# Performance work log

Measured on AMD Instinct MI355X. Metric: run time of the kernel, lower is better.

## Reference

```python
import jax, jax.numpy as jnp
import numpy as np

B, T, C, H = 2, 2048, 1024, 16
HD = C // H  # head dim = 64


def setup_inputs() -> dict:
    key = jax.random.key(0)
    ks = jax.random.split(key, 5)
    scale = 0.02
    return {
        "x": jax.random.normal(ks[0], (B, T, C), dtype=jnp.float32),
        "W_attn": jax.random.normal(ks[1], (C, 3 * C), dtype=jnp.float32) * scale,
        "b_attn": jax.random.normal(ks[2], (3 * C,), dtype=jnp.float32) * scale,
        "W_proj": jax.random.normal(ks[3], (C, C), dtype=jnp.float32) * scale,
        "b_proj": jax.random.normal(ks[4], (C,), dtype=jnp.float32) * scale,
    }


def reference(x, W_attn, b_attn, W_proj, b_proj):
    Bd, Td, Cd = x.shape
    qkv = x @ W_attn + b_attn                      # [B,T,3C]
    q, k, v = jnp.split(qkv, 3, axis=-1)           # each [B,T,C]
    # [B,T,C] -> [B,H,T,HD]
    def heads(t):
        return t.reshape(Bd, Td, H, HD).transpose(0, 2, 1, 3)
    q, k, v = heads(q), heads(k), heads(v)
    att = jnp.einsum('bhqd,bhkd->bhqk', q, k) * (1.0 / np.sqrt(HD))
    causal = jnp.tril(jnp.ones((Td, Td), dtype=bool))
    att = jnp.where(causal[None, None, :, :], att, -jnp.inf)
    att = jax.nn.softmax(att, axis=-1)
    y = jnp.einsum('bhqk,bhkd->bhqd', att, v)      # [B,H,T,HD]
    y = y.transpose(0, 2, 1, 3).reshape(Bd, Td, Cd)
    return y @ W_proj + b_proj
```

## Files before the change

### kernel.cpp

```cpp
#include <hip/hip_runtime.h>
#include <hip/hip_bf16.h>


typedef __attribute__((ext_vector_type(8))) __bf16 bf16x8;
typedef __attribute__((ext_vector_type(8))) short short8;
typedef __attribute__((ext_vector_type(4))) short short4v;
typedef __attribute__((ext_vector_type(4))) float floatx4;

__device__ __forceinline__ unsigned short f2b(float f) {
    unsigned int x = __float_as_uint(f);
    x += 0x7fffu + ((x >> 16) & 1u);
    return (unsigned short)(x >> 16);
}
__device__ __forceinline__ unsigned short f2b_trunc(float f) {
    return (unsigned short)(__float_as_uint(f) >> 16);
}
__device__ __forceinline__ void gld16(const void* g, void* l) {
    __builtin_amdgcn_global_load_lds((const __attribute__((address_space(1))) void*)g,
                                     (__attribute__((address_space(3))) void*)l, 16, 0, 0);
}

__global__ __launch_bounds__(256) void prep_k(
    const float* __restrict__ x,  unsigned short* __restrict__ xb,
    const float* __restrict__ Wa, unsigned short* __restrict__ WTa,
    const float* __restrict__ Wp, unsigned short* __restrict__ WTp)
{
    __shared__ unsigned short tl[64][72];
    const int id = blockIdx.x, t = threadIdx.x;

    if (id < 2048) {
        int i = (id * 256 + t) << 3;
        const float4 a = *(const float4*)(x + i);
        const float4 b = *(const float4*)(x + i + 4);
        short8 v;
        v[0] = (short)f2b(a.x); v[1] = (short)f2b(a.y);
        v[2] = (short)f2b(a.z); v[3] = (short)f2b(a.w);
        v[4] = (short)f2b(b.x); v[5] = (short)f2b(b.y);
        v[6] = (short)f2b(b.z); v[7] = (short)f2b(b.w);
        *(short8*)(xb + i) = v;
        return;
    }

    const float* in;
    unsigned short* out;
    int R, Cc, bx, by;
    if (id < 2816) {
        in = Wa; out = WTa; R = 1024; Cc = 3072;
        bx = (id - 2048) % 48; by = (id - 2048) / 48;
    } else {
        in = Wp; out = WTp; R = 1024; Cc = 1024;
        bx = (id - 2816) % 16; by = (id - 2816) / 16;
    }
    const int r0 = by * 64, c0 = bx * 64;
#pragma unroll
    for (int it = 0; it < 2; ++it) {
        int idx = it * 256 + t, r = idx >> 3, c8 = (idx & 7) << 3;
        const float* p = in + (size_t)(r0 + r) * Cc + c0 + c8;
        const float4 a = *(const float4*)p;
        const float4 b = *(const float4*)(p + 4);
        tl[r][c8 + 0] = f2b(a.x); tl[r][c8 + 1] = f2b(a.y);
        tl[r][c8 + 2] = f2b(a.z); tl[r][c8 + 3] = f2b(a.w);
        tl[r][c8 + 4] = f2b(b.x); tl[r][c8 + 5] = f2b(b.y);
        tl[r][c8 + 6] = f2b(b.z); tl[r][c8 + 7] = f2b(b.w);
    }
    __syncthreads();
#pragma unroll
    for (int it = 0; it < 2; ++it) {
        int idx = it * 256 + t, rr = idx >> 3, c8 = (idx & 7) << 3;
        short8 v;
#pragma unroll
        for (int i = 0; i < 8; ++i) v[i] = (short)tl[c8 + i][rr];
        *(short8*)(out + (size_t)(c0 + rr) * R + r0 + c8) = v;
    }
}

__global__ __launch_bounds__(256) void gemm_qkv(
    const unsigned short* __restrict__ A,
    const unsigned short* __restrict__ BT,
    const float* __restrict__ bias,
    unsigned short* __restrict__ outqk,
    unsigned short* __restrict__ outvt)
{
    __shared__ __align__(16) unsigned short SM[2][2][128][32];
    unsigned short* Esc = &SM[0][0][0][0];

    const int t = threadIdx.x;
    const int w = t >> 6, lane = t & 63, l15 = lane & 15, quad = lane >> 4;
    const int wr = w >> 1, wc = w & 1;
    const int m0 = blockIdx.y * 128, n0 = blockIdx.x * 128;
    const int K = 1024;

    float bia[4];
#pragma unroll
    for (int j = 0; j < 4; ++j) bia[j] = bias[n0 + wc * 64 + j * 16 + l15];

    floatx4 acc[4][4];
#pragma unroll
    for (int i = 0; i < 4; ++i)
#pragma unroll
        for (int j = 0; j < 4; ++j) acc[i][j] = (floatx4)0.f;

    const int row_s = t >> 2, kg_s = (t & 3) << 3;
    const unsigned short* gA = A  + (size_t)(m0 + row_s) * K + kg_s;
    const unsigned short* gB = BT + (size_t)(n0 + row_s) * K + kg_s;
    const int ldst = (w * 64) * 8;

#pragma unroll
    for (int c = 0; c < 2; ++c) {
        gld16(gA + (size_t)c * 64 * K, &SM[0][0][0][0] + c * 2048 + ldst);
        gld16(gB + (size_t)c * 64 * K, &SM[0][1][0][0] + c * 2048 + ldst);
    }

    for (int it = 0; it < 32; ++it) {
        __syncthreads();
        const int cur = it & 1;
        if (it < 31) {
            const int k0 = (it + 1) * 32;
#pragma unroll
            for (int c = 0; c < 2; ++c) {
                gld16(gA + (size_t)c * 64 * K + k0, &SM[cur ^ 1][0][0][0] + c * 2048 + ldst);
                gld16(gB + (size_t)c * 64 * K + k0, &SM[cur ^ 1][1][0][0] + c * 2048 + ldst);
            }
        }
        bf16x8 af[4], bfr[4];
#pragma unroll
        for (int i = 0; i < 4; ++i) af[i] = *(const bf16x8*)&SM[cur][0][wr * 64 + i * 16 + l15][quad * 8];
#pragma unroll
        for (int j = 0; j < 4; ++j) bfr[j] = *(const bf16x8*)&SM[cur][1][wc * 64 + j * 16 + l15][quad * 8];
#pragma unroll
        for (int i = 0; i < 4; ++i)
#pragma unroll
            for (int j = 0; j < 4; ++j)
                acc[i][j] = __builtin_amdgcn_mfma_f32_16x16x32_bf16(af[i], bfr[j], acc[i][j], 0, 0, 0);
    }

    const int bb = m0 >> 11, tbase = m0 & 2047;
    if (n0 < 2048) {
        for (int cf = 0; cf < 2; ++cf) {
            const int fb = n0 + cf * 64;
            const int which = fb >> 10, h = (fb & 1023) >> 6;
            const float scl = (which == 0) ? 0.18033688011112042f : 1.0f;
            __syncthreads();
            if (wc == cf) {
#pragma unroll
                for (int i = 0; i < 4; ++i)
#pragma unroll
                    for (int j = 0; j < 4; ++j)
#pragma unroll
                        for (int r = 0; r < 4; ++r)
                            Esc[(wr * 64 + i * 16 + quad * 4 + r) * 72 + j * 16 + l15] =
                                f2b((acc[i][j][r] + bia[j]) * scl);
            }
            __syncthreads();
            const int row = t >> 1, co = (t & 1) << 5;
            const unsigned short* src = Esc + row * 72 + co;
            unsigned short* dst = outqk + (size_t)which * 4194304
                + (((size_t)(bb * 16 + h) * 2048 + tbase + row) * 64 + co);
#pragma unroll
            for (int u = 0; u < 4; ++u)
                *(short8*)(dst + u * 8) = *(const short8*)(src + u * 8);
        }
    } else {
        const int hb = (n0 & 1023) >> 6;
        for (int hf = 0; hf < 2; ++hf) {
            __syncthreads();
            if (wr == hf) {
#pragma unroll
                for (int i = 0; i < 4; ++i)
#pragma unroll
                    for (int j = 0; j < 4; ++j) {
                        short4v pk;
#pragma unroll
                        for (int r = 0; r < 4; ++r) pk[r] = (short)f2b(acc[i][j][r] + bia[j]);
                        *(short4v*)&Esc[(wc * 64 + j * 16 + l15) * 72 + i * 16 + quad * 4] = pk;
                    }
            }
            __syncthreads();
            const int dl = t >> 1, co = (t & 1) << 5;
            const int h = hb + (dl >> 6), d = dl & 63;
            const unsigned short* src = Esc + dl * 72 + co;
            unsigned short* dst = outvt
                + (((size_t)(bb * 16 + h) * 64 + d) * 2048 + tbase + hf * 64 + co);
#pragma unroll
            for (int u = 0; u < 4; ++u)
                *(short8*)(dst + u * 8) = *(const short8*)(src + u * 8);
        }
    }
}

__global__ __launch_bounds__(256) void gemm_proj(
    const unsigned short* __restrict__ A,
    const unsigned short* __restrict__ BT,
    const float* __restrict__ bias,
    float* __restrict__ outf)
{
    __shared__ __align__(16) unsigned short SM[2][2][128][32];
    float* Ef = (float*)&SM[0][0][0][0];

    const int t = threadIdx.x;
    const int w = t >> 6, lane = t & 63, l15 = lane & 15, quad = lane >> 4;
    const int wr = w >> 1, wc = w & 1;
    const int m0 = blockIdx.y * 128, n0 = blockIdx.x * 128;
    const int K = 1024, N = 1024;

    float bia[4];
#pragma unroll
    for (int j = 0; j < 4; ++j) bia[j] = bias[n0 + wc * 64 + j * 16 + l15];

    floatx4 acc[4][4];
#pragma unroll
    for (int i = 0; i < 4; ++i)
#pragma unroll
        for (int j = 0; j < 4; ++j) acc[i][j] = (floatx4)0.f;

    const int row_s = t >> 2, kg_s = (t & 3) << 3;
    const unsigned short* gA = A  + (size_t)(m0 + row_s) * K + kg_s;
    const unsigned short* gB = BT + (size_t)(n0 + row_s) * K + kg_s;
    const int ldst = (w * 64) * 8;

#pragma unroll
    for (int c = 0; c < 2; ++c) {
        gld16(gA + (size_t)c * 64 * K, &SM[0][0][0][0] + c * 2048 + ldst);
        gld16(gB + (size_t)c * 64 * K, &SM[0][1][0][0] + c * 2048 + ldst);
    }

    for (int it = 0; it < 32; ++it) {
        __syncthreads();
        const int cur = it & 1;
        if (it < 31) {
            const int k0 = (it + 1) * 32;
#pragma unroll
            for (int c = 0; c < 2; ++c) {
                gld16(gA + (size_t)c * 64 * K + k0, &SM[cur ^ 1][0][0][0] + c * 2048 + ldst);
                gld16(gB + (size_t)c * 64 * K + k0, &SM[cur ^ 1][1][0][0] + c * 2048 + ldst);
            }
        }
        bf16x8 af[4], bfr[4];
#pragma unroll
        for (int i = 0; i < 4; ++i) af[i] = *(const bf16x8*)&SM[cur][0][wr * 64 + i * 16 + l15][quad * 8];
#pragma unroll
        for (int j = 0; j < 4; ++j) bfr[j] = *(const bf16x8*)&SM[cur][1][wc * 64 + j * 16 + l15][quad * 8];
#pragma unroll
        for (int i = 0; i < 4; ++i)
#pragma unroll
            for (int j = 0; j < 4; ++j)
                acc[i][j] = __builtin_amdgcn_mfma_f32_16x16x32_bf16(af[i], bfr[j], acc[i][j], 0, 0, 0);
    }

    for (int qf = 0; qf < 4; ++qf) {
        __syncthreads();
        if (wr == (qf >> 1)) {
            const int ib = (qf & 1) * 2;
#pragma unroll
            for (int ii = 0; ii < 2; ++ii)
#pragma unroll
                for (int j = 0; j < 4; ++j)
#pragma unroll
                    for (int r = 0; r < 4; ++r)
                        Ef[(ii * 16 + quad * 4 + r) * 132 + wc * 64 + j * 16 + l15] =
                            acc[ib + ii][j][r] + bia[j];
        }
        __syncthreads();
        const int row = t >> 3, co = (t & 7) << 4;
        const float* src = Ef + row * 132 + co;
        float* dst = outf + (size_t)(m0 + qf * 32 + row) * N + n0 + co;
#pragma unroll
        for (int u = 0; u < 4; ++u)
            *(float4*)(dst + u * 4) = *(const float4*)(src + u * 4);
    }
}

__global__ __launch_bounds__(256) void attn_k(
    const unsigned short* __restrict__ qg,
    const unsigned short* __restrict__ kg,
    const unsigned short* __restrict__ vt,
    unsigned short* __restrict__ y)
{
    __shared__ unsigned short Kb[2][64][64];
    __shared__ unsigned short Vb[2][64][64];
    __shared__ unsigned short Pld[4][16][72];

    const int t = threadIdx.x, w = t >> 6, lane = t & 63;
    const int l15 = lane & 15, quad = lane >> 4;
    const int id = blockIdx.x;
    const int bh = (id & 7) * 4 + ((id >> 3) & 3);
    const int p = id >> 5;
    const int b = bh >> 4, h = bh & 15;

    bf16x8 ones;
#pragma unroll
    for (int i = 0; i < 8; ++i) ones[i] = (__bf16)1.0f;

    const int r_s = t >> 3;
    const int g_s = t & 7;

#pragma unroll 1
    for (int hv = 0; hv < 2; ++hv) {
        const int qt = hv ? (31 - p) : p;
        const int qbase = qt * 64;

        bf16x8 qa[2];
        {
            const unsigned short* qrow = qg + ((size_t)bh * 2048 + qbase + w * 16 + l15) * 64;
            qa[0] = *(const bf16x8*)(qrow + quad * 8);
            qa[1] = *(const bf16x8*)(qrow + 32 + quad * 8);
        }

        floatx4 O[4];
#pragma unroll
        for (int j = 0; j < 4; ++j) O[j] = (floatx4)0.f;
        floatx4 lacc = (floatx4)0.f;

        __syncthreads();
        {
#pragma unroll
            for (int c = 0; c < 2; ++c) {
                int r = c * 32 + r_s;
                int cg = (g_s ^ (r & 7)) << 3;
                gld16(kg + ((size_t)bh * 2048 + r) * 64 + cg,
                      &Kb[0][0][0] + (size_t)(c * 256 + w * 64) * 8);
                gld16(vt + ((size_t)bh * 64 + r) * 2048 + cg,
                      &Vb[0][0][0] + (size_t)(c * 256 + w * 64) * 8);
            }
        }

#pragma unroll 1
        for (int kt = 0; kt <= qt; ++kt) {
            __syncthreads();
            const int cur = kt & 1;
            if (kt < qt) {
                const int kbase = (kt + 1) * 64, nxt = cur ^ 1;
#pragma unroll
                for (int c = 0; c < 2; ++c) {
                    int r = c * 32 + r_s;
                    int cg = (g_s ^ (r & 7)) << 3;
                    gld16(kg + ((size_t)bh * 2048 + kbase + r) * 64 + cg,
                          &Kb[nxt][0][0] + (size_t)(c * 256 + w * 64) * 8);
                    gld16(vt + ((size_t)bh * 64 + r) * 2048 + kbase + cg,
                          &Vb[nxt][0][0] + (size_t)(c * 256 + w * 64) * 8);
                }
            }

            floatx4 sv[4];
#pragma unroll
            for (int jn = 0; jn < 4; ++jn) sv[jn] = (floatx4)0.f;
#pragma unroll
            for (int kk = 0; kk < 2; ++kk) {
#pragma unroll
                for (int jn = 0; jn < 4; ++jn) {
                    bf16x8 bfr = *(const bf16x8*)&Kb[cur][jn * 16 + l15][((kk * 4 + quad) ^ (l15 & 7)) << 3];
                    sv[jn] = __builtin_amdgcn_mfma_f32_16x16x32_bf16(qa[kk], bfr, sv[jn], 0, 0, 0);
                }
            }

            if (kt == qt) {
#pragma unroll
                for (int jn = 0; jn < 4; ++jn) {
                    int key = jn * 16 + l15;
#pragma unroll
                    for (int r = 0; r < 4; ++r) {
                        int qr = w * 16 + quad * 4 + r;
                        sv[jn][r] = exp2f((key > qr) ? -1e30f : sv[jn][r]);
                    }
                }
            } else {
#pragma unroll
                for (int jn = 0; jn < 4; ++jn)
#pragma unroll
                    for (int r = 0; r < 4; ++r) sv[jn][r] = exp2f(sv[jn][r]);
            }

#pragma unroll
            for (int jn = 0; jn < 4; ++jn)
#pragma unroll
                for (int r = 0; r < 4; ++r)
                    Pld[w][quad * 4 + r][jn * 16 + l15] = f2b_trunc(sv[jn][r]);
            __builtin_amdgcn_wave_barrier();
            __builtin_amdgcn_s_waitcnt(0xc07f);
            __builtin_amdgcn_wave_barrier();

#pragma unroll
            for (int kk = 0; kk < 2; ++kk) {
                bf16x8 pa = *(const bf16x8*)&Pld[w][l15][kk * 32 + quad * 8];
                lacc = __builtin_amdgcn_mfma_f32_16x16x32_bf16(pa, ones, lacc, 0, 0, 0);
#pragma unroll
                for (int jd = 0; jd < 4; ++jd) {
                    bf16x8 vb = *(const bf16x8*)&Vb[cur][jd * 16 + l15][((kk * 4 + quad) ^ (l15 & 7)) << 3];
                    O[jd] = __builtin_amdgcn_mfma_f32_16x16x32_bf16(pa, vb, O[jd], 0, 0, 0);
                }
            }
        }

#pragma unroll
        for (int r = 0; r < 4; ++r) {
            float inv = 1.f / lacc[r];
            int tt = qbase + w * 16 + quad * 4 + r;
#pragma unroll
            for (int jd = 0; jd < 4; ++jd) {
                int c = h * 64 + jd * 16 + l15;
                y[((size_t)b * 2048 + tt) * 1024 + c] = f2b(O[jd][r] * inv);
            }
        }
    }
}

extern "C" void kernel_launch(void* const* d_in, const int* in_sizes, int n_in,
                              void* d_out, int out_size, void* d_ws, size_t ws_size,
                              hipStream_t stream) {
    const float* x      = (const float*)d_in[0];
    const float* W_attn = (const float*)d_in[1];
    const float* b_attn = (const float*)d_in[2];
    const float* W_proj = (const float*)d_in[3];
    const float* b_proj = (const float*)d_in[4];
    float* out = (float*)d_out;

    char* ws = (char*)d_ws;
    unsigned short* qk  = (unsigned short*)(ws);
    unsigned short* vtb = (unsigned short*)(ws + 16777216);
    unsigned short* y   = (unsigned short*)(ws + 25165824);
    unsigned short* xb  = (unsigned short*)(ws + 33554432);
    unsigned short* WTa = (unsigned short*)(ws + 41943040);
    unsigned short* WTp = (unsigned short*)(ws + 48234496);

    prep_k<<<3072, 256, 0, stream>>>(x, xb, W_attn, WTa, W_proj, WTp);
    gemm_qkv<<<dim3(24, 32), 256, 0, stream>>>(xb, WTa, b_attn, qk, vtb);
    attn_k<<<512, 256, 0, stream>>>(qk, qk + 4194304, vtb, y);
    gemm_proj<<<dim3(8, 32), 256, 0, stream>>>(y, WTp, b_proj, out);
}
```

Before: 201.1 us.

## Transpose attention scores into registers and run PV in fp16 MFMA

The attention kernel now computes the transposed score tile K·Q^T, so the exponentiated probabilities already sit in the register layout the PV MFMA needs. This removes the per-wave LDS staging buffer and its wait. P and V switch to fp16 with the 16x16x16 f16 MFMA, and the QKV kernel now writes V as fp16 using round-toward-zero pack conversion. Each block now covers 128 contiguous query rows instead of a pair of mirrored 64-row tiles, with the largest-work blocks launched first. The trade-offs are smaller-K MFMAs, a different precision profile for P·V, and possible load imbalance across blocks.

```diff
diff --git a/kernel.cpp b/kernel.cpp
--- a/kernel.cpp
+++ b/kernel.cpp
@@ -6,14 +6,19 @@
 typedef __attribute__((ext_vector_type(8))) short short8;
 typedef __attribute__((ext_vector_type(4))) short short4v;
 typedef __attribute__((ext_vector_type(4))) float floatx4;
+typedef __attribute__((ext_vector_type(2))) __fp16 fp16x2;
+typedef __attribute__((ext_vector_type(4))) _Float16 half4v;
 
 __device__ __forceinline__ unsigned short f2b(float f) {
     unsigned int x = __float_as_uint(f);
     x += 0x7fffu + ((x >> 16) & 1u);
     return (unsigned short)(x >> 16);
 }
-__device__ __forceinline__ unsigned short f2b_trunc(float f) {
-    return (unsigned short)(__float_as_uint(f) >> 16);
+__device__ __forceinline__ half4v pack4h(float a, float b, float c, float d) {
+    union { fp16x2 c2[2]; half4v h4; } u;
+    u.c2[0] = __builtin_amdgcn_cvt_pkrtz(a, b);
+    u.c2[1] = __builtin_amdgcn_cvt_pkrtz(c, d);
+    return u.h4;
 }
 __device__ __forceinline__ void gld16(const void* g, void* l) {
     __builtin_amdgcn_global_load_lds((const __attribute__((address_space(1))) void*)g,
@@ -169,10 +174,9 @@
                 for (int i = 0; i < 4; ++i)
 #pragma unroll
                     for (int j = 0; j < 4; ++j) {
-                        short4v pk;
-#pragma unroll
-                        for (int r = 0; r < 4; ++r) pk[r] = (short)f2b(acc[i][j][r] + bia[j]);
-                        *(short4v*)&Esc[(wc * 64 + j * 16 + l15) * 72 + i * 16 + quad * 4] = pk;
+                        half4v hp = pack4h(acc[i][j][0] + bia[j], acc[i][j][1] + bia[j],
+                                           acc[i][j][2] + bia[j], acc[i][j][3] + bia[j]);
+                        *(half4v*)&Esc[(wc * 64 + j * 16 + l15) * 72 + i * 16 + quad * 4] = hp;
                     }
             }
             __syncthreads();
@@ -278,128 +282,113 @@
 {
     __shared__ unsigned short Kb[2][64][64];
     __shared__ unsigned short Vb[2][64][64];
-    __shared__ unsigned short Pld[4][16][72];
 
     const int t = threadIdx.x, w = t >> 6, lane = t & 63;
     const int l15 = lane & 15, quad = lane >> 4;
     const int id = blockIdx.x;
-    const int bh = (id & 7) * 4 + ((id >> 3) & 3);
-    const int p = id >> 5;
+    const int s = id >> 3;
+    const int bh = (id & 7) * 4 + (s & 3);
+    const int p = 15 - (s >> 2);
     const int b = bh >> 4, h = bh & 15;
-
-    bf16x8 ones;
-#pragma unroll
-    for (int i = 0; i < 8; ++i) ones[i] = (__bf16)1.0f;
-
-    const int r_s = t >> 3;
-    const int g_s = t & 7;
+    const int q0 = p * 128 + w * 32;
+    const int ktend = 2 * p + 2;
+
+    const half4v onesh = {(_Float16)1.f, (_Float16)1.f, (_Float16)1.f, (_Float16)1.f};
+
+    bf16x8 Qf[2][2];
+#pragma unroll
+    for (int qb = 0; qb < 2; ++qb) {
+        const unsigned short* qrow = qg + ((size_t)bh * 2048 + q0 + qb * 16 + l15) * 64 + quad * 8;
+        Qf[qb][0] = *(const bf16x8*)(qrow);
+        Qf[qb][1] = *(const bf16x8*)(qrow + 32);
+    }
+
+    floatx4 OT[2][4];
+#pragma unroll
+    for (int qb = 0; qb < 2; ++qb)
+#pragma unroll
+        for (int jd = 0; jd < 4; ++jd) OT[qb][jd] = (floatx4)0.f;
+    floatx4 lacc[2];
+    lacc[0] = (floatx4)0.f; lacc[1] = (floatx4)0.f;
+
+    const int r_s = t >> 3, g_s = t & 7;
+
+#pragma unroll
+    for (int c = 0; c < 2; ++c) {
+        int r = c * 32 + r_s;
+        int cg = (g_s ^ (r & 7)) << 3;
+        gld16(kg + ((size_t)bh * 2048 + r) * 64 + cg, &Kb[0][0][0] + (size_t)(c * 256 + w * 64) * 8);
+        gld16(vt + ((size_t)bh * 64 + r) * 2048 + cg, &Vb[0][0][0] + (size_t)(c * 256 + w * 64) * 8);
+    }
 
 #pragma unroll 1
-    for (int hv = 0; hv < 2; ++hv) {
-        const int qt = hv ? (31 - p) : p;
-        const int qbase = qt * 64;
-
-        bf16x8 qa[2];
-        {
-            const unsigned short* qrow = qg + ((size_t)bh * 2048 + qbase + w * 16 + l15) * 64;
-            qa[0] = *(const bf16x8*)(qrow + quad * 8);
-            qa[1] = *(const bf16x8*)(qrow + 32 + quad * 8);
-        }
-
-        floatx4 O[4];
-#pragma unroll
-        for (int j = 0; j < 4; ++j) O[j] = (floatx4)0.f;
-        floatx4 lacc = (floatx4)0.f;
-
+    for (int kt = 0; kt < ktend; ++kt) {
         __syncthreads();
-        {
+        const int cur = kt & 1;
+        if (kt + 1 < ktend) {
+            const int kbase = (kt + 1) * 64, nxt = cur ^ 1;
 #pragma unroll
             for (int c = 0; c < 2; ++c) {
                 int r = c * 32 + r_s;
                 int cg = (g_s ^ (r & 7)) << 3;
-                gld16(kg + ((size_t)bh * 2048 + r) * 64 + cg,
-                      &Kb[0][0][0] + (size_t)(c * 256 + w * 64) * 8);
-                gld16(vt + ((size_t)bh * 64 + r) * 2048 + cg,
-                      &Vb[0][0][0] + (size_t)(c * 256 + w * 64) * 8);
-            }
-        }
-
-#pragma unroll 1
-        for (int kt = 0; kt <= qt; ++kt) {
-            __syncthreads();
-            const int cur = kt & 1;
-            if (kt < qt) {
-                const int kbase = (kt + 1) * 64, nxt = cur ^ 1;
-#pragma unroll
-                for (int c = 0; c < 2; ++c) {
-                    int r = c * 32 + r_s;
-                    int cg = (g_s ^ (r & 7)) << 3;
-                    gld16(kg + ((size_t)bh * 2048 + kbase + r) * 64 + cg,
-                          &Kb[nxt][0][0] + (size_t)(c * 256 + w * 64) * 8);
-                    gld16(vt + ((size_t)bh * 64 + r) * 2048 + kbase + cg,
-                          &Vb[nxt][0][0] + (size_t)(c * 256 + w * 64) * 8);
+                gld16(kg + ((size_t)bh * 2048 + kbase + r) * 64 + cg,
+                      &Kb[nxt][0][0] + (size_t)(c * 256 + w * 64) * 8);
+                gld16(vt + ((size_t)bh * 64 + r) * 2048 + kbase + cg,
+                      &Vb[nxt][0][0] + (size_t)(c * 256 + w * 64) * 8);
+            }
+        }
+
+#pragma unroll
+        for (int jk = 0; jk < 4; ++jk) {
+            bf16x8 Kf0 = *(const bf16x8*)&Kb[cur][jk * 16 + l15][((0 * 4 + quad) ^ (l15 & 7)) << 3];
+            bf16x8 Kf1 = *(const bf16x8*)&Kb[cur][jk * 16 + l15][((1 * 4 + quad) ^ (l15 & 7)) << 3];
+            half4v Vf[4];
+#pragma unroll
+            for (int jd = 0; jd < 4; ++jd) {
+                const int pc = ((((2 * jk) + (quad >> 1)) ^ (l15 & 7)) << 3) + (quad & 1) * 4;
+                Vf[jd] = *(const half4v*)&Vb[cur][jd * 16 + l15][pc];
+            }
+
+#pragma unroll
+            for (int qb = 0; qb < 2; ++qb) {
+                const int qlo = q0 + qb * 16;
+                if (kt * 64 > qlo + 15) continue;
+
+                floatx4 st = (floatx4)0.f;
+                st = __builtin_amdgcn_mfma_f32_16x16x32_bf16(Kf0, Qf[qb][0], st, 0, 0, 0);
+                st = __builtin_amdgcn_mfma_f32_16x16x32_bf16(Kf1, Qf[qb][1], st, 0, 0, 0);
+
+                float e[4];
+                const int kb_ = kt * 64 + jk * 16 + quad * 4;
+                const int qg_ = qlo + l15;
+                if (kt * 64 + 63 > qlo) {
+#pragma unroll
+                    for (int r = 0; r < 4; ++r)
+                        e[r] = (kb_ + r > qg_) ? 0.f : exp2f(st[r]);
+                } else {
+#pragma unroll
+                    for (int r = 0; r < 4; ++r) e[r] = exp2f(st[r]);
                 }
-            }
-
-            floatx4 sv[4];
-#pragma unroll
-            for (int jn = 0; jn < 4; ++jn) sv[jn] = (floatx4)0.f;
-#pragma unroll
-            for (int kk = 0; kk < 2; ++kk) {
-#pragma unroll
-                for (int jn = 0; jn < 4; ++jn) {
-                    bf16x8 bfr = *(const bf16x8*)&Kb[cur][jn * 16 + l15][((kk * 4 + quad) ^ (l15 & 7)) << 3];
-                    sv[jn] = __builtin_amdgcn_mfma_f32_16x16x32_bf16(qa[kk], bfr, sv[jn], 0, 0, 0);
-                }
-            }
-
-            if (kt == qt) {
-#pragma unroll
-                for (int jn = 0; jn < 4; ++jn) {
-                    int key = jn * 16 + l15;
-#pragma unroll
-                    for (int r = 0; r < 4; ++r) {
-                        int qr = w * 16 + quad * 4 + r;
-                        sv[jn][r] = exp2f((key > qr) ? -1e30f : sv[jn][r]);
-                    }
-                }
-            } else {
-#pragma unroll
-                for (int jn = 0; jn < 4; ++jn)
-#pragma unroll
-                    for (int r = 0; r < 4; ++r) sv[jn][r] = exp2f(sv[jn][r]);
-            }
-
-#pragma unroll
-            for (int jn = 0; jn < 4; ++jn)
-#pragma unroll
-                for (int r = 0; r < 4; ++r)
-                    Pld[w][quad * 4 + r][jn * 16 + l15] = f2b_trunc(sv[jn][r]);
-            __builtin_amdgcn_wave_barrier();
-            __builtin_amdgcn_s_waitcnt(0xc07f);
-            __builtin_amdgcn_wave_barrier();
-
-#pragma unroll
-            for (int kk = 0; kk < 2; ++kk) {
-                bf16x8 pa = *(const bf16x8*)&Pld[w][l15][kk * 32 + quad * 8];
-                lacc = __builtin_amdgcn_mfma_f32_16x16x32_bf16(pa, ones, lacc, 0, 0, 0);
-#pragma unroll
-                for (int jd = 0; jd < 4; ++jd) {
-                    bf16x8 vb = *(const bf16x8*)&Vb[cur][jd * 16 + l15][((kk * 4 + quad) ^ (l15 & 7)) << 3];
-                    O[jd] = __builtin_amdgcn_mfma_f32_16x16x32_bf16(pa, vb, O[jd], 0, 0, 0);
-                }
-            }
-        }
-
-#pragma unroll
-        for (int r = 0; r < 4; ++r) {
-            float inv = 1.f / lacc[r];
-            int tt = qbase + w * 16 + quad * 4 + r;
-#pragma unroll
-            for (int jd = 0; jd < 4; ++jd) {
-                int c = h * 64 + jd * 16 + l15;
-                y[((size_t)b * 2048 + tt) * 1024 + c] = f2b(O[jd][r] * inv);
-            }
+                half4v Pf = pack4h(e[0], e[1], e[2], e[3]);
+
+                lacc[qb] = __builtin_amdgcn_mfma_f32_16x16x16f16(onesh, Pf, lacc[qb], 0, 0, 0);
+#pragma unroll
+                for (int jd = 0; jd < 4; ++jd)
+                    OT[qb][jd] = __builtin_amdgcn_mfma_f32_16x16x16f16(Vf[jd], Pf, OT[qb][jd], 0, 0, 0);
+            }
+        }
+    }
+
+#pragma unroll
+    for (int qb = 0; qb < 2; ++qb) {
+        const float inv = 1.f / lacc[qb][0];
+        const int q = q0 + qb * 16 + l15;
+#pragma unroll
+        for (int jd = 0; jd < 4; ++jd) {
+            short4v o;
+#pragma unroll
+            for (int r = 0; r < 4; ++r) o[r] = (short)f2b(OT[qb][jd][r] * inv);
+            *(short4v*)(y + ((size_t)b * 2048 + q) * 1024 + h * 64 + jd * 16 + quad * 4) = o;
         }
     }
 }
```

Result: slower. 221.2 us (+10.0%).
